# Optimization experiments

Measured on AMD Instinct MI355X. Metric: run time of the kernel, lower is better.

Reference implementation:

```python
import jax, jax.numpy as jnp
import numpy as np


def _rope(x, fr, fi):
    # Faithful port of apply_rotary_embeddings: deinterleave even/odd elements,
    # reshape to (-1, *fr.shape), rotate, then concat halves and reshape back.
    shp = x.shape
    dims = fr.shape  # (seq_len, 1, head_dim//2)
    xf = x.reshape(-1, 2)
    xr = xf[:, 0].reshape((-1,) + dims)
    xi = xf[:, 1].reshape((-1,) + dims)
    out_r = xr * fr - xi * fi
    out_i = xr * fi + xi * fr
    return jnp.concatenate([out_r, out_i], axis=-1).reshape(shp).astype(x.dtype)


def setup_inputs() -> dict:
    key = jax.random.key(0)
    ks = jax.random.split(key, 9)
    B, S, Dm, H, Hd, P = 16, 1, 4096, 32, 128, 2048
    W = 0.02  # weight scale to keep score magnitudes sane
    return {
        "x": jax.random.normal(ks[0], (B, S, Dm), jnp.float32),
        "cache_k": jax.random.normal(ks[1], (B, P, H, Hd), jnp.float32),
        "cache_v": jax.random.normal(ks[2], (B, P, H, Hd), jnp.float32),
        "freqs_real": jax.random.normal(ks[3], (S, 1, Hd // 2), jnp.float32),
        "freqs_imag": jax.random.normal(ks[4], (S, 1, Hd // 2), jnp.float32),
        "dwq": jax.random.normal(ks[5], (Dm, Dm), jnp.float32) * W,
        "dwk": jax.random.normal(ks[6], (Dm, Dm), jnp.float32) * W,
        "dwv": jax.random.normal(ks[7], (Dm, Dm), jnp.float32) * W,
        "dwo": jax.random.normal(ks[8], (Dm, Dm), jnp.float32) * W,
        "start_pos": P,
    }


def reference(x, cache_k, cache_v, freqs_real, freqs_imag, dwq, dwk, dwv, dwo, start_pos):
    B, S, _ = x.shape
    H, Hd = cache_k.shape[2], cache_k.shape[3]
    scale = 1.0 / np.float32(np.sqrt(Hd))

    xq = (x @ dwq.T).reshape(B, S, H, Hd)
    xk = (x @ dwk.T).reshape(B, S, H, Hd)
    xv = (x @ dwv.T).reshape(B, S, H, Hd)
    xq = _rope(xq, freqs_real, freqs_imag)
    xk = _rope(xk, freqs_real, freqs_imag)

    # KV-cache append (cat-based growth in the original)
    keys = jnp.concatenate([cache_k, xk], axis=1)      # (B, P+S, H, Hd)
    values = jnp.concatenate([cache_v, xv], axis=1)

    q = xq.transpose(0, 2, 1, 3)       # (B, H, S, Hd)
    k = keys.transpose(0, 2, 1, 3)     # (B, H, P+S, Hd)
    v = values.transpose(0, 2, 1, 3)

    scores = jnp.einsum('bhqd,bhkd->bhqk', q, k) * scale
    probs = jax.nn.softmax(scores.astype(jnp.float32), axis=-1).astype(q.dtype)
    out = jnp.einsum('bhqk,bhkd->bhqd', probs, v)
    out = out.transpose(0, 2, 1, 3).reshape(B, S, H * Hd)
    return out @ dwo.T  # allreduce is identity with tp=1
```

## Files before the change

### kernel.cpp

```cpp
#include <hip/hip_runtime.h>
#include <cstdint>

#define DM 4096
#define NB 16
#define NH 32
#define HD 128
#define PP 2048

typedef __attribute__((ext_vector_type(8))) short bf16x8;
typedef __attribute__((ext_vector_type(4))) float f32x4;

__device__ inline short f2bf(float f) {
  uint32_t u = __float_as_uint(f);
  u += 0x7fffu + ((u >> 16) & 1u);
  return (short)(u >> 16);
}

__device__ inline float bf2f(short s) {
  return __uint_as_float(((uint32_t)(uint16_t)s) << 16);
}

__device__ inline void gemv16_block(const float* __restrict__ A,
                                    const float* __restrict__ W,
                                    float* __restrict__ O, int jt) {
  const int wave = threadIdx.x >> 6;
  const int lane = threadIdx.x & 63;
  const int m = lane & 15;
  const int kg = lane >> 4;
  const float* arow = A + (size_t)m * DM;
  const float* wrow = W + (size_t)(jt + m) * DM;
  const int kbase = wave * (DM / 4) + kg * 8;
  f32x4 acc = {0.f, 0.f, 0.f, 0.f};
#pragma unroll 2
  for (int kb = 0; kb < (DM / 4) / 32; ++kb) {
    const int k = kbase + kb * 32;
    float4 xa = *(const float4*)(arow + k);
    float4 xb = *(const float4*)(arow + k + 4);
    float4 wa = *(const float4*)(wrow + k);
    float4 wb = *(const float4*)(wrow + k + 4);
    float xs[8] = {xa.x, xa.y, xa.z, xa.w, xb.x, xb.y, xb.z, xb.w};
    float ws[8] = {wa.x, wa.y, wa.z, wa.w, wb.x, wb.y, wb.z, wb.w};
    bf16x8 ah, al, wh, wl;
#pragma unroll
    for (int i = 0; i < 8; ++i) {
      short h = f2bf(xs[i]);
      ah[i] = h;
      al[i] = f2bf(xs[i] - bf2f(h));
      short g = f2bf(ws[i]);
      wh[i] = g;
      wl[i] = f2bf(ws[i] - bf2f(g));
    }
    acc = __builtin_amdgcn_mfma_f32_16x16x32_bf16(ah, wh, acc, 0, 0, 0);
    acc = __builtin_amdgcn_mfma_f32_16x16x32_bf16(ah, wl, acc, 0, 0, 0);
    acc = __builtin_amdgcn_mfma_f32_16x16x32_bf16(al, wh, acc, 0, 0, 0);
  }
  __shared__ float red[4][256];
  red[wave][lane * 4 + 0] = acc[0];
  red[wave][lane * 4 + 1] = acc[1];
  red[wave][lane * 4 + 2] = acc[2];
  red[wave][lane * 4 + 3] = acc[3];
  __syncthreads();
  const int t = threadIdx.x;
  float s = red[0][t] + red[1][t] + red[2][t] + red[3][t];
  const int l = t >> 2, r = t & 3;
  const int bb = ((l >> 4) << 2) + r;
  const int n = l & 15;
  O[(size_t)bb * DM + jt + n] = s;
}

__global__ __launch_bounds__(256) void qkv_proj_kernel(
    const float* __restrict__ x,
    const float* __restrict__ wq, const float* __restrict__ wk,
    const float* __restrict__ wv,
    float* __restrict__ oq, float* __restrict__ ok, float* __restrict__ ov) {
  const int g = blockIdx.x >> 8;
  const int jt = (blockIdx.x & 255) << 4;
  const float* w = (g == 0) ? wq : (g == 1) ? wk : wv;
  float* o = (g == 0) ? oq : (g == 1) ? ok : ov;
  gemv16_block(x, w, o, jt);
}

__global__ __launch_bounds__(256) void oproj_kernel(
    const float* __restrict__ a, const float* __restrict__ w,
    float* __restrict__ o) {
  gemv16_block(a, w, o, blockIdx.x << 4);
}

__global__ __launch_bounds__(512) void attn_kernel(
    const float* __restrict__ q_raw, const float* __restrict__ k_raw,
    const float* __restrict__ v_raw,
    const float* __restrict__ cache_k, const float* __restrict__ cache_v,
    const float* __restrict__ fr, const float* __restrict__ fi,
    float* __restrict__ attn_out) {
  const int b = blockIdx.x >> 5;
  const int h = blockIdx.x & 31;
  const int t = threadIdx.x;

  __shared__ float q[HD], kn[HD], vn[HD];
  __shared__ float sc[PP + 4];
  __shared__ float pvred[16][HD];
  __shared__ float wredm[8], wreds[8];

  const float* qh = q_raw + (size_t)b * DM + h * HD;
  const float* kh = k_raw + (size_t)b * DM + h * HD;
  const float* vh = v_raw + (size_t)b * DM + h * HD;

  if (t < 64) {
    float f_r = fr[t], f_i = fi[t];
    float qr = qh[2 * t], qi = qh[2 * t + 1];
    float kr = kh[2 * t], ki = kh[2 * t + 1];
    q[t] = qr * f_r - qi * f_i;
    q[t + 64] = qr * f_i + qi * f_r;
    kn[t] = kr * f_r - ki * f_i;
    kn[t + 64] = kr * f_i + ki * f_r;
  } else if (t >= 128 && t < 256) {
    vn[t - 128] = vh[t - 128];
  }
  __syncthreads();

  const float scale = 0.08838834764831845f;
  const float* Kb = cache_k + (size_t)b * (PP * (size_t)DM) + (size_t)h * HD;

  if (t >= 448) {
    const int lane = t - 448;
    float p = q[lane] * kn[lane] + q[lane + 64] * kn[lane + 64];
#pragma unroll
    for (int off = 32; off; off >>= 1) p += __shfl_down(p, off);
    if (lane == 0) sc[PP] = p * scale;
  }

  for (int p = t; p < PP; p += 512) {
    const float* kp = Kb + (size_t)p * DM;
    float acc0 = 0.f, acc1 = 0.f;
#pragma unroll
    for (int d4 = 0; d4 < 64; d4 += 4) {
      float4 k0 = *(const float4*)(kp + d4);
      float4 k1 = *(const float4*)(kp + d4 + 64);
      acc0 += q[d4] * k0.x + q[d4 + 1] * k0.y + q[d4 + 2] * k0.z + q[d4 + 3] * k0.w;
      acc1 += q[d4 + 64] * k1.x + q[d4 + 65] * k1.y + q[d4 + 66] * k1.z + q[d4 + 67] * k1.w;
    }
    sc[p] = (acc0 + acc1) * scale;
  }
  __syncthreads();

  float mloc = -1e30f;
  for (int p = t; p < PP + 1; p += 512) mloc = fmaxf(mloc, sc[p]);
#pragma unroll
  for (int off = 32; off; off >>= 1) mloc = fmaxf(mloc, __shfl_xor(mloc, off));
  if ((t & 63) == 0) wredm[t >> 6] = mloc;
  __syncthreads();
  const float mglob =
      fmaxf(fmaxf(fmaxf(wredm[0], wredm[1]), fmaxf(wredm[2], wredm[3])),
            fmaxf(fmaxf(wredm[4], wredm[5]), fmaxf(wredm[6], wredm[7])));

  float sloc = 0.f;
  for (int p = t; p < PP + 1; p += 512) {
    float e = __expf(sc[p] - mglob);
    sc[p] = e;
    sloc += e;
  }
#pragma unroll
  for (int off = 32; off; off >>= 1) sloc += __shfl_xor(sloc, off);
  if ((t & 63) == 0) wreds[t >> 6] = sloc;
  __syncthreads();
  const float ssum = wreds[0] + wreds[1] + wreds[2] + wreds[3] +
                     wreds[4] + wreds[5] + wreds[6] + wreds[7];
  const float inv = 1.0f / ssum;

  const int g = t >> 5;
  const int dq = (t & 31) << 2;
  const float* Vb = cache_v + (size_t)b * (PP * (size_t)DM) + (size_t)h * HD;
  float4 a0 = {0.f, 0.f, 0.f, 0.f}, a1 = {0.f, 0.f, 0.f, 0.f};
  for (int p = g; p < PP; p += 32) {
    float pr0 = sc[p];
    float4 v0 = *(const float4*)(Vb + (size_t)p * DM + dq);
    a0.x += pr0 * v0.x; a0.y += pr0 * v0.y; a0.z += pr0 * v0.z; a0.w += pr0 * v0.w;
    float pr1 = sc[p + 16];
    float4 v1 = *(const float4*)(Vb + (size_t)(p + 16) * DM + dq);
    a1.x += pr1 * v1.x; a1.y += pr1 * v1.y; a1.z += pr1 * v1.z; a1.w += pr1 * v1.w;
  }
  a0.x += a1.x; a0.y += a1.y; a0.z += a1.z; a0.w += a1.w;
  if (g == 0) {
    float pr = sc[PP];
    a0.x += pr * vn[dq]; a0.y += pr * vn[dq + 1];
    a0.z += pr * vn[dq + 2]; a0.w += pr * vn[dq + 3];
  }
  pvred[g][dq + 0] = a0.x;
  pvred[g][dq + 1] = a0.y;
  pvred[g][dq + 2] = a0.z;
  pvred[g][dq + 3] = a0.w;
  __syncthreads();
  if (t < HD) {
    float o = 0.f;
#pragma unroll
    for (int gg = 0; gg < 16; ++gg) o += pvred[gg][t];
    attn_out[(size_t)b * DM + h * HD + t] = o * inv;
  }
}

extern "C" void kernel_launch(void* const* d_in, const int* in_sizes, int n_in,
                              void* d_out, int out_size, void* d_ws, size_t ws_size,
                              hipStream_t stream) {
  const float* x = (const float*)d_in[0];
  const float* cache_k = (const float*)d_in[1];
  const float* cache_v = (const float*)d_in[2];
  const float* fr = (const float*)d_in[3];
  const float* fi = (const float*)d_in[4];
  const float* dwq = (const float*)d_in[5];
  const float* dwk = (const float*)d_in[6];
  const float* dwv = (const float*)d_in[7];
  const float* dwo = (const float*)d_in[8];
  float* out = (float*)d_out;

  float* qraw = (float*)d_ws;
  float* kraw = qraw + NB * DM;
  float* vraw = kraw + NB * DM;
  float* aout = vraw + NB * DM;

  qkv_proj_kernel<<<768, 256, 0, stream>>>(x, dwq, dwk, dwv, qraw, kraw, vraw);
  attn_kernel<<<512, 512, 0, stream>>>(qraw, kraw, vraw, cache_k, cache_v, fr, fi, aout);
  oproj_kernel<<<256, 256, 0, stream>>>(aout, dwo, out);
}
```

Measured before the change: 290.0 us.

## Split-KV attention with coalesced row reads, fuse RoPE into QKV GEMV

Attention is restructured so each block handles one batch and a 64-row chunk of the KV cache across all 32 heads, reading full contiguous 16KB rows instead of strided 512B per-head slices. A new combine kernel merges the per-chunk partial max, sum and PV results, and adds the new token's contribution. RoPE is fused into the QKV projection epilogue, weight and cache loads use nontemporal hints, and the output projection uses 16 waves per block for more K-parallelism. The cost is an extra kernel launch and a partial-results buffer in workspace.

```diff
diff --git a/kernel.cpp b/kernel.cpp
--- a/kernel.cpp
+++ b/kernel.cpp
@@ -6,6 +6,9 @@
 #define NH 32
 #define HD 128
 #define PP 2048
+#define NCHUNK 32
+#define CROWS 64
+#define PSTRIDE 132
 
 typedef __attribute__((ext_vector_type(8))) short bf16x8;
 typedef __attribute__((ext_vector_type(4))) float f32x4;
@@ -15,187 +18,222 @@
   u += 0x7fffu + ((u >> 16) & 1u);
   return (short)(u >> 16);
 }
-
 __device__ inline float bf2f(short s) {
   return __uint_as_float(((uint32_t)(uint16_t)s) << 16);
 }
-
-__device__ inline void gemv16_block(const float* __restrict__ A,
-                                    const float* __restrict__ W,
-                                    float* __restrict__ O, int jt) {
+__device__ inline f32x4 ntld4(const float* p) {
+  return __builtin_nontemporal_load(reinterpret_cast<const f32x4*>(p));
+}
+
+template <int NW, bool ROPE>
+__device__ inline void gemv16(const float* __restrict__ A,
+                              const float* __restrict__ W,
+                              float* __restrict__ O, int jt,
+                              const float* __restrict__ fr,
+                              const float* __restrict__ fi) {
   const int wave = threadIdx.x >> 6;
   const int lane = threadIdx.x & 63;
   const int m = lane & 15;
   const int kg = lane >> 4;
   const float* arow = A + (size_t)m * DM;
   const float* wrow = W + (size_t)(jt + m) * DM;
-  const int kbase = wave * (DM / 4) + kg * 8;
+  const int kbase = wave * (DM / NW) + kg * 8;
   f32x4 acc = {0.f, 0.f, 0.f, 0.f};
 #pragma unroll 2
-  for (int kb = 0; kb < (DM / 4) / 32; ++kb) {
+  for (int kb = 0; kb < (DM / NW) / 32; ++kb) {
     const int k = kbase + kb * 32;
     float4 xa = *(const float4*)(arow + k);
     float4 xb = *(const float4*)(arow + k + 4);
-    float4 wa = *(const float4*)(wrow + k);
-    float4 wb = *(const float4*)(wrow + k + 4);
+    f32x4 wa = ntld4(wrow + k);
+    f32x4 wb = ntld4(wrow + k + 4);
     float xs[8] = {xa.x, xa.y, xa.z, xa.w, xb.x, xb.y, xb.z, xb.w};
     float ws[8] = {wa.x, wa.y, wa.z, wa.w, wb.x, wb.y, wb.z, wb.w};
     bf16x8 ah, al, wh, wl;
 #pragma unroll
     for (int i = 0; i < 8; ++i) {
-      short h = f2bf(xs[i]);
-      ah[i] = h;
-      al[i] = f2bf(xs[i] - bf2f(h));
-      short g = f2bf(ws[i]);
-      wh[i] = g;
-      wl[i] = f2bf(ws[i] - bf2f(g));
+      short hsh = f2bf(xs[i]);
+      ah[i] = hsh;
+      al[i] = f2bf(xs[i] - bf2f(hsh));
+      short gsh = f2bf(ws[i]);
+      wh[i] = gsh;
+      wl[i] = f2bf(ws[i] - bf2f(gsh));
     }
     acc = __builtin_amdgcn_mfma_f32_16x16x32_bf16(ah, wh, acc, 0, 0, 0);
     acc = __builtin_amdgcn_mfma_f32_16x16x32_bf16(ah, wl, acc, 0, 0, 0);
     acc = __builtin_amdgcn_mfma_f32_16x16x32_bf16(al, wh, acc, 0, 0, 0);
   }
-  __shared__ float red[4][256];
+  __shared__ float red[NW][256];
   red[wave][lane * 4 + 0] = acc[0];
   red[wave][lane * 4 + 1] = acc[1];
   red[wave][lane * 4 + 2] = acc[2];
   red[wave][lane * 4 + 3] = acc[3];
   __syncthreads();
   const int t = threadIdx.x;
-  float s = red[0][t] + red[1][t] + red[2][t] + red[3][t];
-  const int l = t >> 2, r = t & 3;
-  const int bb = ((l >> 4) << 2) + r;
-  const int n = l & 15;
-  O[(size_t)bb * DM + jt + n] = s;
+  float s = 0.f;
+  if (t < 256) {
+#pragma unroll
+    for (int w = 0; w < NW; ++w) s += red[w][t];
+  }
+  float part = 0.f;
+  if (ROPE) {
+    __syncthreads();
+    if (t < 256) red[0][t] = s;
+    __syncthreads();
+    if (t < 256) part = red[0][t ^ 4];
+  }
+  if (t < 256) {
+    const int l = t >> 2, r = t & 3;
+    const int bb = ((l >> 4) << 2) + r;
+    const int n = l & 15;
+    const int c = jt + n;
+    float val;
+    int oc;
+    if (ROPE) {
+      const int j = (c & 127) >> 1;
+      const float f_r = fr[j], f_i = fi[j];
+      if ((c & 1) == 0) {
+        val = s * f_r - part * f_i;
+        oc = (c & ~127) + j;
+      } else {
+        val = part * f_i + s * f_r;
+        oc = (c & ~127) + 64 + j;
+      }
+    } else {
+      val = s;
+      oc = c;
+    }
+    O[(size_t)bb * DM + oc] = val;
+  }
 }
 
 __global__ __launch_bounds__(256) void qkv_proj_kernel(
-    const float* __restrict__ x,
-    const float* __restrict__ wq, const float* __restrict__ wk,
-    const float* __restrict__ wv,
+    const float* __restrict__ x, const float* __restrict__ wq,
+    const float* __restrict__ wk, const float* __restrict__ wv,
+    const float* __restrict__ fr, const float* __restrict__ fi,
     float* __restrict__ oq, float* __restrict__ ok, float* __restrict__ ov) {
   const int g = blockIdx.x >> 8;
   const int jt = (blockIdx.x & 255) << 4;
-  const float* w = (g == 0) ? wq : (g == 1) ? wk : wv;
-  float* o = (g == 0) ? oq : (g == 1) ? ok : ov;
-  gemv16_block(x, w, o, jt);
-}
-
-__global__ __launch_bounds__(256) void oproj_kernel(
+  if (g == 0)
+    gemv16<4, true>(x, wq, oq, jt, fr, fi);
+  else if (g == 1)
+    gemv16<4, true>(x, wk, ok, jt, fr, fi);
+  else
+    gemv16<4, false>(x, wv, ov, jt, nullptr, nullptr);
+}
+
+__global__ __launch_bounds__(1024, 4) void oproj_kernel(
     const float* __restrict__ a, const float* __restrict__ w,
     float* __restrict__ o) {
-  gemv16_block(a, w, o, blockIdx.x << 4);
-}
-
-__global__ __launch_bounds__(512) void attn_kernel(
-    const float* __restrict__ q_raw, const float* __restrict__ k_raw,
-    const float* __restrict__ v_raw,
-    const float* __restrict__ cache_k, const float* __restrict__ cache_v,
-    const float* __restrict__ fr, const float* __restrict__ fi,
-    float* __restrict__ attn_out) {
+  gemv16<16, false>(a, w, o, blockIdx.x << 4, nullptr, nullptr);
+}
+
+__global__ __launch_bounds__(512) void attn_chunk_kernel(
+    const float* __restrict__ qrope, const float* __restrict__ cache_k,
+    const float* __restrict__ cache_v, float* __restrict__ part) {
+  const int b = blockIdx.x >> 5;
+  const int c = blockIdx.x & 31;
+  const int t = threadIdx.x;
+  __shared__ float sc[NH][CROWS];
+
+  const float4 qa = *(const float4*)(qrope + (size_t)b * DM + 4 * t);
+  const float4 qb = *(const float4*)(qrope + (size_t)b * DM + 2048 + 4 * t);
+  const int h1 = t >> 5;
+  const int h2 = h1 + 16;
+  const float scale = 0.08838834764831845f;
+
+  const float* Kb = cache_k + ((size_t)b * PP + (size_t)c * CROWS) * DM;
+#pragma unroll 2
+  for (int r = 0; r < CROWS; ++r) {
+    const float* krow = Kb + (size_t)r * DM + 4 * t;
+    f32x4 k1 = ntld4(krow);
+    f32x4 k2 = ntld4(krow + 2048);
+    float p1 = qa.x * k1.x + qa.y * k1.y + qa.z * k1.z + qa.w * k1.w;
+    float p2 = qb.x * k2.x + qb.y * k2.y + qb.z * k2.z + qb.w * k2.w;
+#pragma unroll
+    for (int off = 1; off <= 16; off <<= 1) {
+      p1 += __shfl_xor(p1, off);
+      p2 += __shfl_xor(p2, off);
+    }
+    if ((t & 31) == 0) {
+      sc[h1][r] = p1 * scale;
+      sc[h2][r] = p2 * scale;
+    }
+  }
+  __syncthreads();
+
+  const int hh = t >> 4, u = t & 15;
+  float4 sv4 = *(const float4*)(&sc[hh][u * 4]);
+  float mx = fmaxf(fmaxf(sv4.x, sv4.y), fmaxf(sv4.z, sv4.w));
+#pragma unroll
+  for (int off = 1; off <= 8; off <<= 1) mx = fmaxf(mx, __shfl_xor(mx, off));
+  float e0 = __expf(sv4.x - mx), e1 = __expf(sv4.y - mx);
+  float e2 = __expf(sv4.z - mx), e3 = __expf(sv4.w - mx);
+  float4 ev = {e0, e1, e2, e3};
+  *(float4*)(&sc[hh][u * 4]) = ev;
+  float sm = (e0 + e1) + (e2 + e3);
+#pragma unroll
+  for (int off = 1; off <= 8; off <<= 1) sm += __shfl_xor(sm, off);
+  float* pb = part + ((size_t)(b * NCHUNK + c) * NH) * PSTRIDE;
+  if (u == 0) {
+    pb[hh * PSTRIDE + 128] = mx;
+    pb[hh * PSTRIDE + 129] = sm;
+  }
+  __syncthreads();
+
+  const float* Vb = cache_v + ((size_t)b * PP + (size_t)c * CROWS) * DM;
+  f32x4 a1 = {0.f, 0.f, 0.f, 0.f}, a2 = {0.f, 0.f, 0.f, 0.f};
+#pragma unroll 2
+  for (int r = 0; r < CROWS; ++r) {
+    const float* vrow = Vb + (size_t)r * DM + 4 * t;
+    f32x4 v1 = ntld4(vrow);
+    f32x4 v2 = ntld4(vrow + 2048);
+    float w1 = sc[h1][r], w2 = sc[h2][r];
+    a1[0] += w1 * v1.x; a1[1] += w1 * v1.y; a1[2] += w1 * v1.z; a1[3] += w1 * v1.w;
+    a2[0] += w2 * v2.x; a2[1] += w2 * v2.y; a2[2] += w2 * v2.z; a2[3] += w2 * v2.w;
+  }
+  const int dbase = (4 * t) & 127;
+  float4 o1 = {a1[0], a1[1], a1[2], a1[3]};
+  float4 o2 = {a2[0], a2[1], a2[2], a2[3]};
+  *(float4*)(pb + h1 * PSTRIDE + dbase) = o1;
+  *(float4*)(pb + h2 * PSTRIDE + dbase) = o2;
+}
+
+__global__ __launch_bounds__(128) void attn_combine_kernel(
+    const float* __restrict__ qrope, const float* __restrict__ krope,
+    const float* __restrict__ vraw, const float* __restrict__ part,
+    float* __restrict__ aout) {
   const int b = blockIdx.x >> 5;
   const int h = blockIdx.x & 31;
-  const int t = threadIdx.x;
-
-  __shared__ float q[HD], kn[HD], vn[HD];
-  __shared__ float sc[PP + 4];
-  __shared__ float pvred[16][HD];
-  __shared__ float wredm[8], wreds[8];
-
-  const float* qh = q_raw + (size_t)b * DM + h * HD;
-  const float* kh = k_raw + (size_t)b * DM + h * HD;
-  const float* vh = v_raw + (size_t)b * DM + h * HD;
-
-  if (t < 64) {
-    float f_r = fr[t], f_i = fi[t];
-    float qr = qh[2 * t], qi = qh[2 * t + 1];
-    float kr = kh[2 * t], ki = kh[2 * t + 1];
-    q[t] = qr * f_r - qi * f_i;
-    q[t + 64] = qr * f_i + qi * f_r;
-    kn[t] = kr * f_r - ki * f_i;
-    kn[t + 64] = kr * f_i + ki * f_r;
-  } else if (t >= 128 && t < 256) {
-    vn[t - 128] = vh[t - 128];
-  }
-  __syncthreads();
-
+  const int d = threadIdx.x;
+  __shared__ float red2[2];
+  __shared__ float mv[NCHUNK], sv[NCHUNK], ec[NCHUNK];
+  const size_t qoff = (size_t)b * DM + h * HD + d;
+  float p = qrope[qoff] * krope[qoff];
+#pragma unroll
+  for (int off = 1; off <= 32; off <<= 1) p += __shfl_xor(p, off);
+  if ((d & 63) == 0) red2[d >> 6] = p;
+  const float* pb = part + ((size_t)b * NCHUNK * NH + h) * PSTRIDE;
+  if (d < NCHUNK) {
+    mv[d] = pb[(size_t)d * NH * PSTRIDE + 128];
+    sv[d] = pb[(size_t)d * NH * PSTRIDE + 129];
+  }
+  __syncthreads();
   const float scale = 0.08838834764831845f;
-  const float* Kb = cache_k + (size_t)b * (PP * (size_t)DM) + (size_t)h * HD;
-
-  if (t >= 448) {
-    const int lane = t - 448;
-    float p = q[lane] * kn[lane] + q[lane + 64] * kn[lane + 64];
-#pragma unroll
-    for (int off = 32; off; off >>= 1) p += __shfl_down(p, off);
-    if (lane == 0) sc[PP] = p * scale;
-  }
-
-  for (int p = t; p < PP; p += 512) {
-    const float* kp = Kb + (size_t)p * DM;
-    float acc0 = 0.f, acc1 = 0.f;
-#pragma unroll
-    for (int d4 = 0; d4 < 64; d4 += 4) {
-      float4 k0 = *(const float4*)(kp + d4);
-      float4 k1 = *(const float4*)(kp + d4 + 64);
-      acc0 += q[d4] * k0.x + q[d4 + 1] * k0.y + q[d4 + 2] * k0.z + q[d4 + 3] * k0.w;
-      acc1 += q[d4 + 64] * k1.x + q[d4 + 65] * k1.y + q[d4 + 66] * k1.z + q[d4 + 67] * k1.w;
-    }
-    sc[p] = (acc0 + acc1) * scale;
-  }
-  __syncthreads();
-
-  float mloc = -1e30f;
-  for (int p = t; p < PP + 1; p += 512) mloc = fmaxf(mloc, sc[p]);
-#pragma unroll
-  for (int off = 32; off; off >>= 1) mloc = fmaxf(mloc, __shfl_xor(mloc, off));
-  if ((t & 63) == 0) wredm[t >> 6] = mloc;
-  __syncthreads();
-  const float mglob =
-      fmaxf(fmaxf(fmaxf(wredm[0], wredm[1]), fmaxf(wredm[2], wredm[3])),
-            fmaxf(fmaxf(wredm[4], wredm[5]), fmaxf(wredm[6], wredm[7])));
-
-  float sloc = 0.f;
-  for (int p = t; p < PP + 1; p += 512) {
-    float e = __expf(sc[p] - mglob);
-    sc[p] = e;
-    sloc += e;
-  }
-#pragma unroll
-  for (int off = 32; off; off >>= 1) sloc += __shfl_xor(sloc, off);
-  if ((t & 63) == 0) wreds[t >> 6] = sloc;
-  __syncthreads();
-  const float ssum = wreds[0] + wreds[1] + wreds[2] + wreds[3] +
-                     wreds[4] + wreds[5] + wreds[6] + wreds[7];
-  const float inv = 1.0f / ssum;
-
-  const int g = t >> 5;
-  const int dq = (t & 31) << 2;
-  const float* Vb = cache_v + (size_t)b * (PP * (size_t)DM) + (size_t)h * HD;
-  float4 a0 = {0.f, 0.f, 0.f, 0.f}, a1 = {0.f, 0.f, 0.f, 0.f};
-  for (int p = g; p < PP; p += 32) {
-    float pr0 = sc[p];
-    float4 v0 = *(const float4*)(Vb + (size_t)p * DM + dq);
-    a0.x += pr0 * v0.x; a0.y += pr0 * v0.y; a0.z += pr0 * v0.z; a0.w += pr0 * v0.w;
-    float pr1 = sc[p + 16];
-    float4 v1 = *(const float4*)(Vb + (size_t)(p + 16) * DM + dq);
-    a1.x += pr1 * v1.x; a1.y += pr1 * v1.y; a1.z += pr1 * v1.z; a1.w += pr1 * v1.w;
-  }
-  a0.x += a1.x; a0.y += a1.y; a0.z += a1.z; a0.w += a1.w;
-  if (g == 0) {
-    float pr = sc[PP];
-    a0.x += pr * vn[dq]; a0.y += pr * vn[dq + 1];
-    a0.z += pr * vn[dq + 2]; a0.w += pr * vn[dq + 3];
-  }
-  pvred[g][dq + 0] = a0.x;
-  pvred[g][dq + 1] = a0.y;
-  pvred[g][dq + 2] = a0.z;
-  pvred[g][dq + 3] = a0.w;
-  __syncthreads();
-  if (t < HD) {
-    float o = 0.f;
-#pragma unroll
-    for (int gg = 0; gg < 16; ++gg) o += pvred[gg][t];
-    attn_out[(size_t)b * DM + h * HD + t] = o * inv;
-  }
+  const float snew = (red2[0] + red2[1]) * scale;
+  float M = snew;
+#pragma unroll
+  for (int c = 0; c < NCHUNK; ++c) M = fmaxf(M, mv[c]);
+  if (d < NCHUNK) ec[d] = __expf(mv[d] - M);
+  __syncthreads();
+  const float en = __expf(snew - M);
+  float S = en;
+  float acc = en * vraw[qoff];
+#pragma unroll 4
+  for (int c = 0; c < NCHUNK; ++c) {
+    acc += ec[c] * pb[(size_t)c * NH * PSTRIDE + d];
+    S += ec[c] * sv[c];
+  }
+  aout[qoff] = acc / S;
 }
 
 extern "C" void kernel_launch(void* const* d_in, const int* in_sizes, int n_in,
@@ -212,12 +250,15 @@
   const float* dwo = (const float*)d_in[8];
   float* out = (float*)d_out;
 
-  float* qraw = (float*)d_ws;
-  float* kraw = qraw + NB * DM;
-  float* vraw = kraw + NB * DM;
+  float* qrope = (float*)d_ws;
+  float* krope = qrope + NB * DM;
+  float* vraw = krope + NB * DM;
   float* aout = vraw + NB * DM;
-
-  qkv_proj_kernel<<<768, 256, 0, stream>>>(x, dwq, dwk, dwv, qraw, kraw, vraw);
-  attn_kernel<<<512, 512, 0, stream>>>(qraw, kraw, vraw, cache_k, cache_v, fr, fi, aout);
-  oproj_kernel<<<256, 256, 0, stream>>>(aout, dwo, out);
-}
+  float* part = aout + NB * DM;
+
+  qkv_proj_kernel<<<768, 256, 0, stream>>>(x, dwq, dwk, dwv, fr, fi,
+                                           qrope, krope, vraw);
+  attn_chunk_kernel<<<512, 512, 0, stream>>>(qrope, cache_k, cache_v, part);
+  attn_combine_kernel<<<512, 128, 0, stream>>>(qrope, krope, vraw, part, aout);
+  oproj_kernel<<<256, 1024, 0, stream>>>(aout, dwo, out);
+}
```

Result: faster. 246.3 us (-15.1%).
